# Kernel tuning notes

Hardware: AMD Instinct MI355X
Metric: run time of the kernel (lower is better)

Reference implementation:

```python
import jax, jax.numpy as jnp
import numpy as np

B, C, CO, H, W = 64, 64, 64, 56, 56
E, K = 8, 2


def _conv3x3(x, k, b):
    # x: [B,C,H,W], k: [CO,C,3,3], b: [CO]
    y = jax.lax.conv_general_dilated(
        x, k, window_strides=(1, 1), padding='SAME',
        dimension_numbers=('NCHW', 'OIHW', 'NCHW'))
    return y + b[None, :, None, None]


def setup_inputs() -> dict:
    key = jax.random.key(0)
    k1, k2, k3, k4, k5 = jax.random.split(key, 5)
    x = jax.random.normal(k1, (B, C, H, W), dtype=jnp.float32)
    weights = jax.random.uniform(k2, (B, K), dtype=jnp.float32)
    indices = jax.random.randint(k3, (B, K), 0, E, dtype=jnp.int32)
    W_exp = jax.random.normal(k4, (E, CO, C, 3, 3), dtype=jnp.float32) * 0.05
    b_exp = jax.random.normal(k5, (E, CO), dtype=jnp.float32) * 0.01
    return {'x': x, 'weights': weights, 'indices': indices,
            'W_exp': W_exp, 'b_exp': b_exp}


def reference(x, weights, indices, W_exp, b_exp):
    # Dense-equivalent MoE dispatch: run every expert on the full batch,
    # then gather the top-k expert outputs per sample and combine.
    # Same math as the masked gather / index_add_ loop in the torch module.
    # acts: [E, B, CO, H, W]
    acts = jax.vmap(lambda k, b: jax.nn.relu(_conv3x3(x, k, b)))(W_exp, b_exp)
    acts_b = jnp.transpose(acts, (1, 0, 2, 3, 4))  # [B, E, CO, H, W]
    idx = indices[:, :, None, None, None].astype(jnp.int32)
    sel = jnp.take_along_axis(acts_b, idx, axis=1)  # [B, K, CO, H, W]
    out = jnp.sum(sel * weights[:, :, None, None, None], axis=1)  # [B, CO, H, W]
    return out
```

## Files before the change

### kernel.cpp

```cpp
#include <hip/hip_runtime.h>


#define BB 64
#define CC 64
#define COO 64
#define HH 56
#define WW 56

typedef __bf16 bf16x8 __attribute__((ext_vector_type(8)));
typedef float  f32x4  __attribute__((ext_vector_type(4)));

__global__ __launch_bounds__(256) void prep_kernel(
    const float* __restrict__ x, const float* __restrict__ Wexp,
    __bf16* __restrict__ xT, __bf16* __restrict__ Wpack)
{
    const int bx  = blockIdx.x;
    const int tid = threadIdx.x;

    if (bx < 960) {
        __shared__ float tile[CC][WW + 1];
        const int b   = bx / 15;
        const int grp = bx - b * 15;
        #pragma unroll 1
        for (int rr = 0; rr < 4; ++rr) {
            const int hp = grp * 4 + rr;
            if (hp >= 58) break;
            __bf16* dst = xT + ((size_t)b * 58 + hp) * 66 * CC;
            const bool interior = (hp >= 1 && hp <= HH);
            if (!interior) {
                bf16x8 z = {};
                for (int j = tid; j < 66 * CC / 8; j += 256)
                    *(bf16x8*)(dst + j * 8) = z;
                continue;
            }
            const int h = hp - 1;
            const float* xb = x + (size_t)b * CC * HH * WW + (size_t)h * WW;
            for (int i = tid; i < CC * 14; i += 256) {
                const int c = i / 14, wq = i - c * 14;
                const float4 f = *(const float4*)(xb + (size_t)c * HH * WW + wq * 4);
                tile[c][wq * 4 + 0] = f.x; tile[c][wq * 4 + 1] = f.y;
                tile[c][wq * 4 + 2] = f.z; tile[c][wq * 4 + 3] = f.w;
            }
            __syncthreads();
            for (int j = tid; j < 66 * 8; j += 256) {
                const int wc = j >> 3, cg = j & 7;
                bf16x8 v = {};
                if (wc >= 1 && wc <= WW) {
                    const int w = wc - 1;
                    #pragma unroll
                    for (int u = 0; u < 8; ++u)
                        v[u] = (__bf16)tile[cg * 8 + u][w];
                }
                *(bf16x8*)(dst + wc * CC + cg * 8) = v;
            }
            __syncthreads();
        }
    } else {
        const int wp = bx - 960;
        const int e  = wp / 9, rs = wp - e * 9;
        const int r  = rs / 3, s  = rs - r * 3;
        for (int idx = tid; idx < 4096; idx += 256) {
            const int ks   = idx >> 11;
            const int rem  = idx & 2047;
            const int mt   = rem >> 9;
            const int lane = (rem >> 3) & 63;
            const int j    = idx & 7;
            const int co = mt * 16 + (lane & 15);
            const int c  = ks * 32 + ((lane >> 4) << 3) + j;
            const float v = Wexp[((((size_t)e * COO + co) * CC + c) * 3 + r) * 3 + s];
            Wpack[(size_t)e * 36864 + (size_t)rs * 4096 + idx] = (__bf16)v;
        }
    }
}

__global__ __launch_bounds__(256, 2) void moe_conv_mfma(
    const __bf16* __restrict__ xT, const __bf16* __restrict__ Wpack,
    const float* __restrict__ gate_w, const int* __restrict__ gate_i,
    const float* __restrict__ bexp, float* __restrict__ out)
{
    __shared__ __bf16 ldsA[2 * 12288];

    const int b   = blockIdx.y;
    const int h0  = blockIdx.x * 4;
    const int tid = threadIdx.x;
    const int wid = tid >> 6, lane = tid & 63;
    const int n15 = lane & 15, quad = lane >> 4;
    const int wcol = wid * 16 + n15;

    const int   e0 = gate_i[b * 2 + 0], e1 = gate_i[b * 2 + 1];
    const float g0 = gate_w[b * 2 + 0], g1 = gate_w[b * 2 + 1];

    const __bf16* xb = xT + (size_t)b * 58 * 66 * CC;

    f32x4 acc[2][4][4] = {};

    for (int r = 0; r < 3; ++r) {
        __syncthreads();
        {
            const __bf16* s0 = Wpack + (size_t)e0 * 36864 + r * 12288;
            const __bf16* s1 = Wpack + (size_t)e1 * 36864 + r * 12288;
            #pragma unroll
            for (int i = 0; i < 12; ++i) {
                const int q    = wid * 12 + i;
                const int slot = q >= 24;
                const int rem  = q - slot * 24;
                const __bf16* src = (slot ? s1 : s0) + rem * 512 + lane * 8;
                const uint4 tmp = *(const uint4*)src;
                *(uint4*)&ldsA[q * 512 + lane * 8] = tmp;
            }
        }
        __syncthreads();

        #pragma unroll
        for (int s = 0; s < 3; ++s) {
            #pragma unroll
            for (int ks = 0; ks < 2; ++ks) {
                bf16x8 bf[4];
                #pragma unroll
                for (int t = 0; t < 4; ++t) {
                    const int hr1 = h0 + t + r;
                    const int wc1 = wcol + s;
                    bf[t] = *(const bf16x8*)(
                        xb + (size_t)(hr1 * 66 + wc1) * CC + ks * 32 + quad * 8);
                }
                #pragma unroll
                for (int slot = 0; slot < 2; ++slot) {
                    #pragma unroll
                    for (int mt = 0; mt < 4; ++mt) {
                        const bf16x8 af = *(const bf16x8*)
                            &ldsA[slot * 12288 + (s * 2 + ks) * 2048 + mt * 512 + lane * 8];
                        #pragma unroll
                        for (int t = 0; t < 4; ++t)
                            acc[slot][mt][t] = __builtin_amdgcn_mfma_f32_16x16x32_bf16(
                                af, bf[t], acc[slot][mt][t], 0, 0, 0);
                    }
                }
            }
        }
    }

    if (wcol < WW) {
        #pragma unroll
        for (int t = 0; t < 4; ++t) {
            const int h = h0 + t;
            #pragma unroll
            for (int mt = 0; mt < 4; ++mt) {
                #pragma unroll
                for (int v = 0; v < 4; ++v) {
                    const int co = mt * 16 + quad * 4 + v;
                    float a0 = acc[0][mt][t][v] + bexp[e0 * COO + co];
                    float a1 = acc[1][mt][t][v] + bexp[e1 * COO + co];
                    a0 = fmaxf(a0, 0.f);
                    a1 = fmaxf(a1, 0.f);
                    out[(((size_t)b * COO + co) * HH + h) * WW + wcol] =
                        g0 * a0 + g1 * a1;
                }
            }
        }
    }
}

extern "C" void kernel_launch(void* const* d_in, const int* in_sizes, int n_in,
                              void* d_out, int out_size, void* d_ws, size_t ws_size,
                              hipStream_t stream) {
    const float* x      = (const float*)d_in[0];
    const float* gate_w = (const float*)d_in[1];
    const int*   gate_i = (const int*)  d_in[2];
    const float* Wexp   = (const float*)d_in[3];
    const float* bexp   = (const float*)d_in[4];
    float* out = (float*)d_out;

    __bf16* Wpack = (__bf16*)d_ws;
    __bf16* xT    = (__bf16*)((char*)d_ws + 589824);

    prep_kernel<<<dim3(1032), 256, 0, stream>>>(x, Wexp, xT, Wpack);
    moe_conv_mfma<<<dim3(14, BB), 256, 0, stream>>>(xT, Wpack, gate_w, gate_i,
                                                    bexp, out);
}
```

Measured before the change: 162.0 us.

## Split output channels across blocks and restructure loop over K-halves and taps

Each block now computes half of the output channels (32 instead of 64), which halves the accumulator registers and doubles the grid. The reduction loop is reordered to iterate over two channel halves, staging all nine taps' weights for that half into a smaller LDS buffer, with launch bounds raised to allow four blocks per CU. The intent is higher occupancy and more parallelism to hide global loads of the input tile. The cost is that every input fragment is now fetched from global memory by two blocks instead of one, and the tap loop is not unrolled.

```diff
diff --git a/kernel.cpp b/kernel.cpp
--- a/kernel.cpp
+++ b/kernel.cpp
@@ -73,15 +73,17 @@
     }
 }
 
-__global__ __launch_bounds__(256, 2) void moe_conv_mfma(
+__global__ __launch_bounds__(256, 4) void moe_conv_mfma(
     const __bf16* __restrict__ xT, const __bf16* __restrict__ Wpack,
     const float* __restrict__ gate_w, const int* __restrict__ gate_i,
     const float* __restrict__ bexp, float* __restrict__ out)
 {
-    __shared__ __bf16 ldsA[2 * 12288];
+    __shared__ __bf16 ldsA[18432];
 
+    const int bx  = blockIdx.x;
     const int b   = blockIdx.y;
-    const int h0  = blockIdx.x * 4;
+    const int hg  = bx >> 1, coh = bx & 1;
+    const int h0  = hg * 4;
     const int tid = threadIdx.x;
     const int wid = tid >> 6, lane = tid & 63;
     const int n15 = lane & 15, quad = lane >> 4;
@@ -90,50 +92,48 @@
     const int   e0 = gate_i[b * 2 + 0], e1 = gate_i[b * 2 + 1];
     const float g0 = gate_w[b * 2 + 0], g1 = gate_w[b * 2 + 1];
 
-    const __bf16* xb = xT + (size_t)b * 58 * 66 * CC;
+    const __bf16* s0p = Wpack + (size_t)e0 * 36864;
+    const __bf16* s1p = Wpack + (size_t)e1 * 36864;
+    const __bf16* xb  = xT + (size_t)b * 58 * 66 * CC;
 
-    f32x4 acc[2][4][4] = {};
+    f32x4 acc[2][2][4] = {};
 
-    for (int r = 0; r < 3; ++r) {
+    #pragma unroll 1
+    for (int ks = 0; ks < 2; ++ks) {
         __syncthreads();
-        {
-            const __bf16* s0 = Wpack + (size_t)e0 * 36864 + r * 12288;
-            const __bf16* s1 = Wpack + (size_t)e1 * 36864 + r * 12288;
-            #pragma unroll
-            for (int i = 0; i < 12; ++i) {
-                const int q    = wid * 12 + i;
-                const int slot = q >= 24;
-                const int rem  = q - slot * 24;
-                const __bf16* src = (slot ? s1 : s0) + rem * 512 + lane * 8;
-                const uint4 tmp = *(const uint4*)src;
-                *(uint4*)&ldsA[q * 512 + lane * 8] = tmp;
-            }
+        #pragma unroll
+        for (int i = 0; i < 9; ++i) {
+            const int q    = wid * 9 + i;
+            const int slot = q / 18;
+            const int rem  = q - slot * 18;
+            const int tap  = rem >> 1, mtl = rem & 1;
+            const __bf16* src = (slot ? s1p : s0p)
+                + (size_t)tap * 4096 + ks * 2048 + (coh * 2 + mtl) * 512 + lane * 8;
+            *(uint4*)&ldsA[q * 512 + lane * 8] = *(const uint4*)src;
         }
         __syncthreads();
 
-        #pragma unroll
-        for (int s = 0; s < 3; ++s) {
+        #pragma unroll 1
+        for (int tap = 0; tap < 9; ++tap) {
+            const int r = tap / 3, s = tap - r * 3;
+            bf16x8 bfr[4];
             #pragma unroll
-            for (int ks = 0; ks < 2; ++ks) {
-                bf16x8 bf[4];
+            for (int t = 0; t < 4; ++t) {
+                const int hr1 = h0 + t + r;
+                const int wc1 = wcol + s;
+                bfr[t] = *(const bf16x8*)(
+                    xb + (size_t)(hr1 * 66 + wc1) * CC + ks * 32 + quad * 8);
+            }
+            #pragma unroll
+            for (int slot = 0; slot < 2; ++slot) {
                 #pragma unroll
-                for (int t = 0; t < 4; ++t) {
-                    const int hr1 = h0 + t + r;
-                    const int wc1 = wcol + s;
-                    bf[t] = *(const bf16x8*)(
-                        xb + (size_t)(hr1 * 66 + wc1) * CC + ks * 32 + quad * 8);
-                }
-                #pragma unroll
-                for (int slot = 0; slot < 2; ++slot) {
+                for (int mtl = 0; mtl < 2; ++mtl) {
+                    const bf16x8 af = *(const bf16x8*)
+                        &ldsA[(size_t)((slot * 18 + tap * 2 + mtl) * 512 + lane * 8)];
                     #pragma unroll
-                    for (int mt = 0; mt < 4; ++mt) {
-                        const bf16x8 af = *(const bf16x8*)
-                            &ldsA[slot * 12288 + (s * 2 + ks) * 2048 + mt * 512 + lane * 8];
-                        #pragma unroll
-                        for (int t = 0; t < 4; ++t)
-                            acc[slot][mt][t] = __builtin_amdgcn_mfma_f32_16x16x32_bf16(
-                                af, bf[t], acc[slot][mt][t], 0, 0, 0);
-                    }
+                    for (int t = 0; t < 4; ++t)
+                        acc[slot][mtl][t] = __builtin_amdgcn_mfma_f32_16x16x32_bf16(
+                            af, bfr[t], acc[slot][mtl][t], 0, 0, 0);
                 }
             }
         }
@@ -144,12 +144,12 @@
         for (int t = 0; t < 4; ++t) {
             const int h = h0 + t;
             #pragma unroll
-            for (int mt = 0; mt < 4; ++mt) {
+            for (int mtl = 0; mtl < 2; ++mtl) {
                 #pragma unroll
                 for (int v = 0; v < 4; ++v) {
-                    const int co = mt * 16 + quad * 4 + v;
-                    float a0 = acc[0][mt][t][v] + bexp[e0 * COO + co];
-                    float a1 = acc[1][mt][t][v] + bexp[e1 * COO + co];
+                    const int co = coh * 32 + mtl * 16 + quad * 4 + v;
+                    float a0 = acc[0][mtl][t][v] + bexp[e0 * COO + co];
+                    float a1 = acc[1][mtl][t][v] + bexp[e1 * COO + co];
                     a0 = fmaxf(a0, 0.f);
                     a1 = fmaxf(a1, 0.f);
                     out[(((size_t)b * COO + co) * HH + h) * WW + wcol] =
@@ -174,6 +174,6 @@
     __bf16* xT    = (__bf16*)((char*)d_ws + 589824);
 
     prep_kernel<<<dim3(1032), 256, 0, stream>>>(x, Wexp, xT, Wpack);
-    moe_conv_mfma<<<dim3(14, BB), 256, 0, stream>>>(xT, Wpack, gate_w, gate_i,
+    moe_conv_mfma<<<dim3(28, BB), 256, 0, stream>>>(xT, Wpack, gate_w, gate_i,
                                                     bexp, out);
 }
```

Result: slower. 183.8 us (+13.5%).
